# Performance work log

Measured on AMD Instinct MI355X. Metric: run time of the kernel, lower is better.

The kernel has to match this reference:

```python
import jax, jax.numpy as jnp
import numpy as np

SEQ = 2048
DIM = 4096
N_HEADS = 32
N_KV_HEADS = 8
HEAD_DIM = DIM // N_HEADS  # 128
ROPE_THETA = 500000.0


def setup_inputs() -> dict:
    key = jax.random.key(0)
    ks = jax.random.split(key, 5)
    s = 0.02  # keep activations numerically tame
    return {
        "x": jax.random.normal(ks[0], (SEQ, DIM), dtype=jnp.float32),
        "wq": jax.random.normal(ks[1], (DIM, DIM), dtype=jnp.float32) * s,
        "wk": jax.random.normal(ks[2], (N_KV_HEADS * HEAD_DIM, DIM), dtype=jnp.float32) * s,
        "wv": jax.random.normal(ks[3], (N_KV_HEADS * HEAD_DIM, DIM), dtype=jnp.float32) * s,
        "wo": jax.random.normal(ks[4], (DIM, DIM), dtype=jnp.float32) * s,
    }


def _rope(t):
    # t: [S, H, D]; pairs (t[...,2i], t[...,2i+1]) rotated by angle pos * theta^(-i/(D/2)),
    # matching torch.view_as_complex on x.view(S, -1, 2) * polar(1, pos*freq).
    S, H, D = t.shape
    half = D // 2
    freqs = 1.0 / (ROPE_THETA ** (jnp.arange(half, dtype=jnp.float32) / half))
    ang = jnp.arange(S, dtype=jnp.float32)[:, None] * freqs[None, :]  # [S, half]
    cos = jnp.cos(ang)[:, None, :]  # [S, 1, half]
    sin = jnp.sin(ang)[:, None, :]
    tr = t.reshape(S, H, half, 2)
    x0, x1 = tr[..., 0], tr[..., 1]
    r0 = x0 * cos - x1 * sin
    r1 = x0 * sin + x1 * cos
    return jnp.stack([r0, r1], axis=-1).reshape(S, H, D)


def reference(x, wq, wk, wv, wo):
    S = x.shape[0]
    group = N_HEADS // N_KV_HEADS
    # Per-head projections (batched over heads instead of python loop)
    q = jnp.einsum("sd,hkd->shk", x, wq.reshape(N_HEADS, HEAD_DIM, DIM))        # [S,H,D]
    k = jnp.einsum("sd,hkd->shk", x, wk.reshape(N_KV_HEADS, HEAD_DIM, DIM))     # [S,Hkv,D]
    v = jnp.einsum("sd,hkd->shk", x, wv.reshape(N_KV_HEADS, HEAD_DIM, DIM))     # [S,Hkv,D]
    q = _rope(q)
    k = _rope(k)
    # GQA: q head h uses kv head h // group -> repeat kv heads consecutively
    kf = jnp.repeat(k, group, axis=1)  # [S,H,D]
    vf = jnp.repeat(v, group, axis=1)  # [S,H,D]
    scores = jnp.einsum("shd,thd->hst", q, kf) / jnp.sqrt(jnp.float32(HEAD_DIM))
    causal = jnp.tril(jnp.ones((S, S), dtype=bool))
    scores = jnp.where(causal[None], scores, -jnp.inf)
    probs = jax.nn.softmax(scores, axis=-1)
    out = jnp.einsum("hst,thd->shd", probs, vf).reshape(S, N_HEADS * HEAD_DIM)
    return out @ wo.T
```

## Files before the change

### kernel.cpp

```cpp
#include <hip/hip_runtime.h>
#include <stdint.h>

#define SEQ   2048
#define DIM   4096
#define NHEAD 32
#define NKV   8
#define HD    128
#define KVDIM (NKV*HD)

typedef __bf16 bf16x8 __attribute__((ext_vector_type(8)));
typedef float  f32x4  __attribute__((ext_vector_type(4)));

__device__ __forceinline__ uint16_t f2bf(float f) {
  uint32_t u = __float_as_uint(f);
  uint32_t r = (u + 0x7FFFu + ((u >> 16) & 1u)) >> 16;
  return (uint16_t)r;
}
__device__ __forceinline__ float bf2f(uint16_t h) {
  return __uint_as_float(((uint32_t)h) << 16);
}
__device__ __forceinline__ bf16x8 ld_frag(const uint16_t* p) {
  return *(const bf16x8*)p;
}
__device__ __forceinline__ void async_cp16(const void* g, void* lds) {
  __builtin_amdgcn_global_load_lds(
      (const __attribute__((address_space(1))) void*)g,
      (__attribute__((address_space(3))) void*)lds, 16, 0, 0);
}

__global__ __launch_bounds__(256) void k_conv(const float* __restrict__ s,
                                              uint16_t* __restrict__ d, int n4) {
  int i = blockIdx.x * 256 + threadIdx.x;
  if (i >= n4) return;
  const float4 v = ((const float4*)s)[i];
  ushort4 o;
  o.x = f2bf(v.x); o.y = f2bf(v.y); o.z = f2bf(v.z); o.w = f2bf(v.w);
  ((ushort4*)d)[i] = o;
}

__device__ __forceinline__ void store_c(float* p, float v)    { *p = v; }
__device__ __forceinline__ void store_c(uint16_t* p, float v) { *p = f2bf(v); }

template <typename OT>
__device__ __forceinline__ void gemm_nt_body(
    const uint16_t* __restrict__ A, const uint16_t* __restrict__ B,
    OT* __restrict__ C, int ldC, int m0, int n0)
{
  __shared__ __align__(16) uint16_t sA[128 * 32];
  __shared__ __align__(16) uint16_t sB[128 * 32];
  const int tid  = threadIdx.x;
  const int lane = tid & 63;
  const int wv   = tid >> 6;
  const int quad = lane >> 4;
  const int l16  = lane & 15;
  const int wm   = (wv & 1) << 6;
  const int wn   = (wv >> 1) << 6;

  const int p0 = tid, p1 = tid + 256;
  const int r0 = p0 >> 2, c0 = (p0 & 3) ^ ((r0 >> 1) & 3);
  const int r1 = p1 >> 2, c1 = (p1 & 3) ^ ((r1 >> 1) & 3);

  const uint16_t* gA0 = A + (size_t)(m0 + r0) * DIM + c0 * 8;
  const uint16_t* gA1 = A + (size_t)(m0 + r1) * DIM + c1 * 8;
  const uint16_t* gB0 = B + (size_t)(n0 + r0) * DIM + c0 * 8;
  const uint16_t* gB1 = B + (size_t)(n0 + r1) * DIM + c1 * 8;
  uint16_t* lA0 = sA + p0 * 8;
  uint16_t* lA1 = sA + p1 * 8;
  uint16_t* lB0 = sB + p0 * 8;
  uint16_t* lB1 = sB + p1 * 8;

  f32x4 acc[4][4] = {};

  int offA[4], offB[4];
  #pragma unroll
  for (int t = 0; t < 4; t++) {
    int ml = wm + t * 16 + l16;
    offA[t] = (ml * 4 + (quad ^ ((ml >> 1) & 3))) * 8;
    int nl = wn + t * 16 + l16;
    offB[t] = (nl * 4 + (quad ^ ((nl >> 1) & 3))) * 8;
  }

  for (int k0 = 0; k0 < DIM; k0 += 32) {
    async_cp16(gA0 + k0, lA0);
    async_cp16(gA1 + k0, lA1);
    async_cp16(gB0 + k0, lB0);
    async_cp16(gB1 + k0, lB1);
    __syncthreads();
    bf16x8 af[4], bfv[4];
    #pragma unroll
    for (int t = 0; t < 4; t++) {
      af[t]  = ld_frag(sA + offA[t]);
      bfv[t] = ld_frag(sB + offB[t]);
    }
    #pragma unroll
    for (int mt = 0; mt < 4; mt++)
      #pragma unroll
      for (int nt = 0; nt < 4; nt++)
        acc[mt][nt] = __builtin_amdgcn_mfma_f32_16x16x32_bf16(af[mt], bfv[nt], acc[mt][nt], 0, 0, 0);
    __syncthreads();
  }

  #pragma unroll
  for (int mt = 0; mt < 4; mt++)
    #pragma unroll
    for (int nt = 0; nt < 4; nt++)
      #pragma unroll
      for (int r = 0; r < 4; r++) {
        int row = m0 + wm + mt * 16 + quad * 4 + r;
        int col = n0 + wn + nt * 16 + l16;
        store_c(&C[(size_t)row * ldC + col], acc[mt][nt][r]);
      }
}

__global__ __launch_bounds__(256) void k_gemm_q(const uint16_t* __restrict__ xb,
                                                const uint16_t* __restrict__ wqb,
                                                uint16_t* __restrict__ Qb) {
  gemm_nt_body<uint16_t>(xb, wqb, Qb, DIM, blockIdx.y * 128, blockIdx.x * 128);
}
__global__ __launch_bounds__(256) void k_gemm_kv(const uint16_t* __restrict__ xb,
                                                 const uint16_t* __restrict__ wkb,
                                                 const uint16_t* __restrict__ wvb,
                                                 uint16_t* __restrict__ Kb,
                                                 uint16_t* __restrict__ Vb) {
  int bx = blockIdx.x;
  const uint16_t* Bp = (bx < 8) ? wkb : wvb;
  uint16_t* Cp = (bx < 8) ? Kb : Vb;
  gemm_nt_body<uint16_t>(xb, Bp, Cp, KVDIM, blockIdx.y * 128, (bx & 7) * 128);
}
__global__ __launch_bounds__(256) void k_gemm_o(const uint16_t* __restrict__ ab,
                                                const uint16_t* __restrict__ wob,
                                                float* __restrict__ out) {
  gemm_nt_body<float>(ab, wob, out, DIM, blockIdx.y * 128, blockIdx.x * 128);
}

__global__ __launch_bounds__(256) void k_rope(uint16_t* __restrict__ Qb,
                                              uint16_t* __restrict__ Kb) {
  int idx = blockIdx.x * 256 + threadIdx.x;
  int i = idx & 63;
  int rem = idx >> 6;
  int head = rem % (NHEAD + NKV);
  int s = rem / (NHEAD + NKV);
  float ang = (float)s * expf(-0.20503693f * (float)i);
  float sn, cs;
  sincosf(ang, &sn, &cs);
  uint16_t* p;
  if (head < NHEAD) p = Qb + (size_t)s * DIM + head * HD + 2 * i;
  else              p = Kb + (size_t)s * KVDIM + (head - NHEAD) * HD + 2 * i;
  float x0 = bf2f(p[0]), x1 = bf2f(p[1]);
  p[0] = f2bf(x0 * cs - x1 * sn);
  p[1] = f2bf(x0 * sn + x1 * cs);
}

__global__ __launch_bounds__(256) void k_vtrans(const uint16_t* __restrict__ Vb,
                                                uint16_t* __restrict__ VT) {
  __shared__ uint16_t t[64][72];
  const int s0 = blockIdx.x * 64;
  const int c0 = blockIdx.y * 64;
  const int tid = threadIdx.x;
  #pragma unroll
  for (int i = 0; i < 2; i++) {
    int idx = i * 256 + tid;
    int r = idx >> 3, ch = idx & 7;
    uint4 dv = *(const uint4*)(Vb + (size_t)(s0 + r) * KVDIM + c0 + ch * 8);
    *(uint4*)(&t[r][ch * 8]) = dv;
  }
  __syncthreads();
  const int kvh = c0 >> 7;
  const int dbase = c0 & 127;
  #pragma unroll
  for (int i = 0; i < 2; i++) {
    int idx = i * 256 + tid;
    int d = idx >> 3, sc = idx & 7;
    uint16_t tmp[8];
    #pragma unroll
    for (int j2 = 0; j2 < 8; j2++) tmp[j2] = t[sc * 8 + j2][d];
    *(uint4*)(VT + (size_t)kvh * HD * SEQ + (size_t)(dbase + d) * SEQ + s0 + sc * 8) = *(const uint4*)tmp;
  }
}

#define BKV 64
__global__ __launch_bounds__(256) void k_flash(
    const uint16_t* __restrict__ Qb, const uint16_t* __restrict__ Kb,
    const uint16_t* __restrict__ VT, uint16_t* __restrict__ Ob)
{
  const int qt  = 15 - (int)blockIdx.x;
  const int h   = blockIdx.y;
  const int kvh = h >> 2;
  const int tid = threadIdx.x;
  const int lane = tid & 63;
  const int wv  = tid >> 6;
  const int quad = lane >> 4;
  const int l16 = lane & 15;
  const int q0 = qt * 128;

  __shared__ __align__(16) uint16_t sK[BKV * 128];
  __shared__ __align__(16) uint16_t sVT[HD * BKV];
  __shared__ __align__(16) uint16_t sP[4 * 32 * 72];

  const uint16_t* Kbase  = Kb + kvh * HD;
  const uint16_t* VTbase = VT + (size_t)kvh * HD * SEQ;

  bf16x8 qf[2][4];
  #pragma unroll
  for (int mt = 0; mt < 2; mt++)
    #pragma unroll
    for (int ks = 0; ks < 4; ks++)
      qf[mt][ks] = ld_frag(Qb + (size_t)(q0 + wv * 32 + mt * 16 + l16) * DIM + h * HD + ks * 32 + quad * 8);

  f32x4 Oacc[2][8] = {};
  float mrow[2][4], lrow[2][4];
  #pragma unroll
  for (int mt = 0; mt < 2; mt++)
    #pragma unroll
    for (int r = 0; r < 4; r++) { mrow[mt][r] = -3.0e38f; lrow[mt][r] = 0.0f; }

  const float scale = 0.08838834764831845f;
  const int njt = 2 * (qt + 1);

  for (int j = 0; j < njt; j++) {
    const int t0 = j * BKV;
    #pragma unroll
    for (int i = 0; i < 4; i++) {
      int pos = i * 256 + tid;
      int row = pos >> 4, g = (pos & 15) ^ (row & 7);
      async_cp16(Kbase + (size_t)(t0 + row) * KVDIM + g * 8, sK + pos * 8);
      int vrow = pos >> 3, vg = (pos & 7) ^ (vrow & 7);
      async_cp16(VTbase + (size_t)vrow * SEQ + t0 + vg * 8, sVT + pos * 8);
    }
    __syncthreads();

    bool active = (t0 <= q0 + wv * 32 + 31);
    if (active) {
      f32x4 Sacc[2][4] = {};
      #pragma unroll
      for (int ks = 0; ks < 4; ks++) {
        bf16x8 kf[4];
        #pragma unroll
        for (int nt = 0; nt < 4; nt++)
          kf[nt] = ld_frag(sK + (nt * 16 + l16) * 128 + (((ks * 4 + quad) ^ (l16 & 7)) * 8));
        #pragma unroll
        for (int mt = 0; mt < 2; mt++)
          #pragma unroll
          for (int nt = 0; nt < 4; nt++)
            Sacc[mt][nt] = __builtin_amdgcn_mfma_f32_16x16x32_bf16(qf[mt][ks], kf[nt], Sacc[mt][nt], 0, 0, 0);
      }
      const bool diag = (t0 + BKV - 1) > (q0 + wv * 32);
      #pragma unroll
      for (int mt = 0; mt < 2; mt++)
        #pragma unroll
        for (int nt = 0; nt < 4; nt++)
          #pragma unroll
          for (int r = 0; r < 4; r++) {
            float sv = Sacc[mt][nt][r] * scale;
            if (diag) {
              int qg = q0 + wv * 32 + mt * 16 + quad * 4 + r;
              int tg = t0 + nt * 16 + l16;
              if (tg > qg) sv = -3.0e38f;
            }
            Sacc[mt][nt][r] = sv;
          }
      float alpha[2][4];
      #pragma unroll
      for (int mt = 0; mt < 2; mt++)
        #pragma unroll
        for (int r = 0; r < 4; r++) {
          float mx = Sacc[mt][0][r];
          #pragma unroll
          for (int nt = 1; nt < 4; nt++) mx = fmaxf(mx, Sacc[mt][nt][r]);
          #pragma unroll
          for (int sh = 1; sh < 16; sh <<= 1) mx = fmaxf(mx, __shfl_xor(mx, sh, 64));
          float mnew = fmaxf(mrow[mt][r], mx);
          float al = __expf(mrow[mt][r] - mnew);
          mrow[mt][r] = mnew;
          float sum = 0.0f;
          #pragma unroll
          for (int nt = 0; nt < 4; nt++) {
            float pv = __expf(Sacc[mt][nt][r] - mnew);
            Sacc[mt][nt][r] = pv;
            sum += pv;
          }
          #pragma unroll
          for (int sh = 1; sh < 16; sh <<= 1) sum += __shfl_xor(sum, sh, 64);
          lrow[mt][r] = lrow[mt][r] * al + sum;
          alpha[mt][r] = al;
        }
      #pragma unroll
      for (int mt = 0; mt < 2; mt++)
        #pragma unroll
        for (int nt = 0; nt < 4; nt++)
          #pragma unroll
          for (int r = 0; r < 4; r++)
            sP[(wv * 32 + mt * 16 + quad * 4 + r) * 72 + nt * 16 + l16] = f2bf(Sacc[mt][nt][r]);
      #pragma unroll
      for (int mt = 0; mt < 2; mt++)
        #pragma unroll
        for (int dt = 0; dt < 8; dt++)
          #pragma unroll
          for (int r = 0; r < 4; r++)
            Oacc[mt][dt][r] *= alpha[mt][r];
      #pragma unroll
      for (int ks = 0; ks < 2; ks++) {
        bf16x8 pf[2], vf[8];
        #pragma unroll
        for (int mt = 0; mt < 2; mt++)
          pf[mt] = ld_frag(sP + (wv * 32 + mt * 16 + l16) * 72 + ks * 32 + quad * 8);
        #pragma unroll
        for (int dt = 0; dt < 8; dt++)
          vf[dt] = ld_frag(sVT + (dt * 16 + l16) * 64 + (((ks * 4 + quad) ^ (l16 & 7)) * 8));
        #pragma unroll
        for (int mt = 0; mt < 2; mt++)
          #pragma unroll
          for (int dt = 0; dt < 8; dt++)
            Oacc[mt][dt] = __builtin_amdgcn_mfma_f32_16x16x32_bf16(pf[mt], vf[dt], Oacc[mt][dt], 0, 0, 0);
      }
    }
    __syncthreads();
  }

  #pragma unroll
  for (int mt = 0; mt < 2; mt++)
    #pragma unroll
    for (int r = 0; r < 4; r++) {
      float inv = 1.0f / lrow[mt][r];
      size_t row = q0 + wv * 32 + mt * 16 + quad * 4 + r;
      #pragma unroll
      for (int dt = 0; dt < 8; dt++)
        Ob[row * DIM + h * HD + dt * 16 + l16] = f2bf(Oacc[mt][dt][r] * inv);
    }
}

extern "C" void kernel_launch(void* const* d_in, const int* in_sizes, int n_in,
                              void* d_out, int out_size, void* d_ws, size_t ws_size,
                              hipStream_t stream) {
  const float* x  = (const float*)d_in[0];
  const float* wq = (const float*)d_in[1];
  const float* wk = (const float*)d_in[2];
  const float* wv = (const float*)d_in[3];
  const float* wo = (const float*)d_in[4];
  float* out = (float*)d_out;

  uint8_t* ws = (uint8_t*)d_ws;
  uint16_t* xb    = (uint16_t*)(ws + 0);
  uint16_t* wbig  = (uint16_t*)(ws + 16777216ull);
  uint16_t* wkb   = (uint16_t*)(ws + 50331648ull);
  uint16_t* wvb   = (uint16_t*)(ws + 58720256ull);
  uint16_t* Qb    = (uint16_t*)(ws + 67108864ull);
  uint16_t* Kb    = (uint16_t*)(ws + 83886080ull);
  uint16_t* Vb    = (uint16_t*)(ws + 88080384ull);
  uint16_t* attnb = xb;
  uint16_t* VT    = wbig;

  k_conv<<<8192, 256, 0, stream>>>(x, xb, 2097152);
  k_conv<<<16384, 256, 0, stream>>>(wq, wbig, 4194304);
  k_gemm_q<<<dim3(32, 16), 256, 0, stream>>>(xb, wbig, Qb);
  k_conv<<<4096, 256, 0, stream>>>(wk, wkb, 1048576);
  k_conv<<<4096, 256, 0, stream>>>(wv, wvb, 1048576);
  k_gemm_kv<<<dim3(16, 16), 256, 0, stream>>>(xb, wkb, wvb, Kb, Vb);
  k_vtrans<<<dim3(32, 16), 256, 0, stream>>>(Vb, VT);
  k_rope<<<20480, 256, 0, stream>>>(Qb, Kb);
  k_flash<<<dim3(16, 32), 256, 0, stream>>>(Qb, Kb, VT, attnb);
  k_conv<<<16384, 256, 0, stream>>>(wo, wbig, 4194304);
  k_gemm_o<<<dim3(32, 16), 256, 0, stream>>>(attnb, wbig, out);
}
```

Before: 690.9 us.

## Split causal flash attention over KV segments and merge with a combine kernel

The flash attention kernel now splits each query tile's KV range into segments of up to 8 KV tiles. Each block handles one (query tile, segment) pair, ordered longest-first through a constant table. Each block writes its unnormalized partial output in bf16 plus per-row max and sum, and a new combine kernel merges the segments with log-sum-exp weights. The aim is to even out the causal load imbalance and fill more CUs (1280 blocks instead of 512), at the cost of an extra launch, partial-output traffic, and bf16 rounding of the unnormalized partials.

```diff
diff --git a/kernel.cpp b/kernel.cpp
--- a/kernel.cpp
+++ b/kernel.cpp
@@ -179,19 +179,32 @@
 }
 
 #define BKV 64
-__global__ __launch_bounds__(256) void k_flash(
+#define NPAIR 40
+__device__ __constant__ uint8_t c_pair[NPAIR] = {
+  12,16,20,24,28,29,32,33,36,37,40,41,44,45,46,48,49,50,52,53,54,56,57,58,60,61,62,63,
+  8,25,42,59,
+  4,21,38,55,
+  0,17,34,51
+};
+__device__ __constant__ uint8_t c_base[16] = {0,1,2,3,4,6,8,10,12,15,18,21,24,28,32,36};
+
+__global__ __launch_bounds__(256) void k_flash_split(
     const uint16_t* __restrict__ Qb, const uint16_t* __restrict__ Kb,
-    const uint16_t* __restrict__ VT, uint16_t* __restrict__ Ob)
+    const uint16_t* __restrict__ VT, uint16_t* __restrict__ Opart,
+    float* __restrict__ ml)
 {
-  const int qt  = 15 - (int)blockIdx.x;
-  const int h   = blockIdx.y;
-  const int kvh = h >> 2;
-  const int tid = threadIdx.x;
+  const int pair = c_pair[blockIdx.x];
+  const int qt   = pair >> 2;
+  const int seg  = pair & 3;
+  const int h    = blockIdx.y;
+  const int kvh  = h >> 2;
+  const int slot = h * NPAIR + c_base[qt] + seg;
+  const int tid  = threadIdx.x;
   const int lane = tid & 63;
-  const int wv  = tid >> 6;
+  const int wv   = tid >> 6;
   const int quad = lane >> 4;
-  const int l16 = lane & 15;
-  const int q0 = qt * 128;
+  const int l16  = lane & 15;
+  const int q0   = qt * 128;
 
   __shared__ __align__(16) uint16_t sK[BKV * 128];
   __shared__ __align__(16) uint16_t sVT[HD * BKV];
@@ -215,9 +228,10 @@
     for (int r = 0; r < 4; r++) { mrow[mt][r] = -3.0e38f; lrow[mt][r] = 0.0f; }
 
   const float scale = 0.08838834764831845f;
-  const int njt = 2 * (qt + 1);
-
-  for (int j = 0; j < njt; j++) {
+  const int j0 = seg * 8;
+  const int j1 = min(j0 + 8, 2 * (qt + 1));
+
+  for (int j = j0; j < j1; j++) {
     const int t0 = j * BKV;
     #pragma unroll
     for (int i = 0; i < 4; i++) {
@@ -317,16 +331,72 @@
     __syncthreads();
   }
 
+  uint16_t* Op = Opart + (size_t)slot * (128 * 128);
   #pragma unroll
   for (int mt = 0; mt < 2; mt++)
     #pragma unroll
     for (int r = 0; r < 4; r++) {
-      float inv = 1.0f / lrow[mt][r];
-      size_t row = q0 + wv * 32 + mt * 16 + quad * 4 + r;
+      int row = wv * 32 + mt * 16 + quad * 4 + r;
       #pragma unroll
       for (int dt = 0; dt < 8; dt++)
-        Ob[row * DIM + h * HD + dt * 16 + l16] = f2bf(Oacc[mt][dt][r] * inv);
-    }
+        Op[row * 128 + dt * 16 + l16] = f2bf(Oacc[mt][dt][r]);
+      if (l16 == 0) {
+        ml[(size_t)slot * 256 + row * 2]     = mrow[mt][r];
+        ml[(size_t)slot * 256 + row * 2 + 1] = lrow[mt][r];
+      }
+    }
+}
+
+__global__ __launch_bounds__(256) void k_combine(
+    const uint16_t* __restrict__ Opart, const float* __restrict__ ml,
+    uint16_t* __restrict__ attnb)
+{
+  const int qt = blockIdx.x;
+  const int h  = blockIdx.y;
+  const int nseg = (qt >> 2) + 1;
+  const int slot0 = h * NPAIR + c_base[qt];
+  const int tid = threadIdx.x;
+  const int row = tid >> 1;
+  const int dh  = (tid & 1) * 64;
+
+  float m_i[4], w[4];
+  float mstar = -3.0e38f;
+  #pragma unroll
+  for (int i = 0; i < 4; i++) {
+    if (i < nseg) {
+      m_i[i] = ml[(size_t)(slot0 + i) * 256 + row * 2];
+      mstar = fmaxf(mstar, m_i[i]);
+    }
+  }
+  float L = 0.0f;
+  #pragma unroll
+  for (int i = 0; i < 4; i++) {
+    if (i < nseg) {
+      float li = ml[(size_t)(slot0 + i) * 256 + row * 2 + 1];
+      w[i] = __expf(m_i[i] - mstar);
+      L += w[i] * li;
+    } else w[i] = 0.0f;
+  }
+  const float invL = 1.0f / L;
+
+  uint16_t* dst = attnb + (size_t)(qt * 128 + row) * DIM + h * HD + dh;
+  #pragma unroll
+  for (int c = 0; c < 8; c++) {
+    int d = dh + c * 8;
+    float acc[8] = {};
+    #pragma unroll
+    for (int i = 0; i < 4; i++) {
+      if (i < nseg) {
+        bf16x8 v = ld_frag(Opart + (size_t)(slot0 + i) * (128 * 128) + row * 128 + d);
+        #pragma unroll
+        for (int j = 0; j < 8; j++) acc[j] += w[i] * (float)v[j];
+      }
+    }
+    uint16_t outv[8];
+    #pragma unroll
+    for (int j = 0; j < 8; j++) outv[j] = f2bf(acc[j] * invL);
+    *(uint4*)(dst + c * 8) = *(const uint4*)outv;
+  }
 }
 
 extern "C" void kernel_launch(void* const* d_in, const int* in_sizes, int n_in,
@@ -348,7 +418,9 @@
   uint16_t* Kb    = (uint16_t*)(ws + 83886080ull);
   uint16_t* Vb    = (uint16_t*)(ws + 88080384ull);
   uint16_t* attnb = xb;
-  uint16_t* VT    = wbig;
+  uint16_t* Opart = (uint16_t*)(ws + 16777216ull);
+  float*    mlbuf = (float*)(ws + 58720256ull);
+  uint16_t* VT    = (uint16_t*)(ws + 62914560ull);
 
   k_conv<<<8192, 256, 0, stream>>>(x, xb, 2097152);
   k_conv<<<16384, 256, 0, stream>>>(wq, wbig, 4194304);
@@ -358,7 +430,8 @@
   k_gemm_kv<<<dim3(16, 16), 256, 0, stream>>>(xb, wkb, wvb, Kb, Vb);
   k_vtrans<<<dim3(32, 16), 256, 0, stream>>>(Vb, VT);
   k_rope<<<20480, 256, 0, stream>>>(Qb, Kb);
-  k_flash<<<dim3(16, 32), 256, 0, stream>>>(Qb, Kb, VT, attnb);
+  k_flash_split<<<dim3(NPAIR, 32), 256, 0, stream>>>(Qb, Kb, VT, Opart, mlbuf);
+  k_combine<<<dim3(16, 32), 256, 0, stream>>>(Opart, mlbuf, attnb);
   k_conv<<<16384, 256, 0, stream>>>(wo, wbig, 4194304);
   k_gemm_o<<<dim3(32, 16), 256, 0, stream>>>(attnb, wbig, out);
 }
```

After: 683.9 us. No clear change (-1.0%).
